# Kernel optimization log

Hardware: AMD Instinct MI355X
Metric: run time of the kernel (lower is better)

The kernel has to match this reference:

```python
import jax, jax.numpy as jnp
import numpy as np

THRESHOLD = 1.25
CURRENT_DECAY = 0.25
VOLTAGE_DECAY = 0.03
B, C_IN, C_HID, C_OUT, T = 16, 64 * 64 * 2, 512, 100, 300


def weight_norm(v, g):
    # per-output-neuron weight normalization: w = g * v / ||v||
    return g[:, None] * v / jnp.linalg.norm(v, axis=1, keepdims=True)


def spike_fn(volt):
    return (volt >= THRESHOLD).astype(volt.dtype)


def lif(z, cd, vd):
    # z: [B, C, T]  CUBA leaky integrate-and-fire recurrence over time
    zT = jnp.moveaxis(z, -1, 0)  # [T, B, C]
    zero = jnp.zeros_like(zT[0])

    def step(carry, zt):
        cur, volt = carry
        cur = (1.0 - cd) * cur + zt
        volt = (1.0 - vd) * volt + cur
        s = spike_fn(volt)
        volt = volt * (1.0 - s)  # reset on spike
        return (cur, volt), s

    _, sT = jax.lax.scan(step, (zero, zero), zT)
    return jnp.moveaxis(sT, 0, -1)  # [B, C, T]


def setup_inputs() -> dict:
    key = jax.random.key(0)
    ks = jax.random.split(key, 8)
    spike = (jax.random.uniform(ks[0], (B, C_IN, T)) < 0.02).astype(jnp.float32)
    s = 0.05
    return {
        "spike": spike,
        "v1": jax.random.normal(ks[1], (C_HID, C_IN), jnp.float32) * s,
        "g1": jnp.ones((C_HID,), jnp.float32),
        "v2": jax.random.normal(ks[2], (C_HID, C_HID), jnp.float32) * s,
        "g2": jnp.ones((C_HID,), jnp.float32),
        "v3": jax.random.normal(ks[3], (C_OUT, C_HID), jnp.float32) * s,
        "g3": jnp.ones((C_OUT,), jnp.float32),
        "current_decays": jnp.full((3,), CURRENT_DECAY, jnp.float32),
        "voltage_decays": jnp.full((3,), VOLTAGE_DECAY, jnp.float32),
    }


def reference(spike, v1, g1, v2, g2, v3, g3, current_decays, voltage_decays):
    x = spike
    for i, (v, g) in enumerate(((v1, g1), (v2, g2), (v3, g3))):
        w = weight_norm(v, g)                      # [out, in]
        z = jnp.einsum("oi,bit->bot", w, x)        # synapse
        x = lif(z, current_decays[i], voltage_decays[i])  # CUBA neuron
    return x
```

## Files before the change

kernel.cpp:

```cpp
#include <hip/hip_runtime.h>
#include <stdint.h>
#include <math.h>

#define NB   16
#define CIN  8192
#define CHID 512
#define COUT 100
#define TT   300
#define TG4  4
#define NTG4 75
#define NW1  256
#define EVCAP1 384
#define EVCAP2 512

__global__ void norm_kernel(const float* __restrict__ v, float* __restrict__ nrm, int cin) {
    int row = blockIdx.x;
    const float* vr = v + (size_t)row * cin;
    float s = 0.f;
    for (int i = threadIdx.x; i < cin; i += 256) {
        float x = vr[i];
        s = __fadd_rn(s, __fmul_rn(x, x));
    }
    __shared__ float red[256];
    red[threadIdx.x] = s;
    __syncthreads();
    for (int off = 128; off > 0; off >>= 1) {
        if (threadIdx.x < off) red[threadIdx.x] += red[threadIdx.x + off];
        __syncthreads();
    }
    if (threadIdx.x == 0) nrm[row] = sqrtf(red[0]);
}

template<int WS>
__global__ void trans_kernel(const float* __restrict__ v, const float* __restrict__ g,
                             const float* __restrict__ nrm, float* __restrict__ wt,
                             int RO, int CI) {
    __shared__ float tile[32][33];
    int i0 = blockIdx.x * 32, o0 = blockIdx.y * 32;
    int tx = threadIdx.x, ty = threadIdx.y;
    for (int k = 0; k < 32; k += 8) {
        int o = o0 + ty + k, i = i0 + tx;
        float val = 0.f;
        if (o < RO) val = __fmul_rn(v[(size_t)o * CI + i], g[o]) / nrm[o];
        tile[ty + k][tx] = val;
    }
    __syncthreads();
    for (int k = 0; k < 32; k += 8) {
        int i = i0 + ty + k, oo = o0 + tx;
        if (oo < WS) wt[(size_t)i * WS + oo] = tile[tx][ty + k];
    }
}

__global__ __launch_bounds__(256) void mask_kernel(const float* __restrict__ spike,
                                                   uint32_t* __restrict__ maskT) {
    __shared__ uint32_t flag[64][16];
    int b = blockIdx.x, itile = blockIdx.y;
    int tid = threadIdx.x;
    int row = tid >> 2, qc = tid & 3;
    const float* sp = spike + ((size_t)(b * CIN + itile * 64 + row)) * TT;
    for (int tc = 0; tc < 5; ++tc) {
        #pragma unroll
        for (int k = 0; k < 4; ++k) {
            int t0 = tc * 64 + k * 16 + qc * 4;
            uint32_t packed = 0;
            if (t0 + 3 < TT) {
                float4 v = *(const float4*)(sp + t0);
                packed = (v.x != 0.f ? 1u : 0u) | (v.y != 0.f ? 0x100u : 0u)
                       | (v.z != 0.f ? 0x10000u : 0u) | (v.w != 0.f ? 0x1000000u : 0u);
            }
            flag[row][k * 4 + qc] = packed;
        }
        __syncthreads();
        if (tid < 128) {
            int t_l = tid >> 1, half = tid & 1;
            int t = tc * 64 + t_l;
            if (t < TT) {
                uint32_t word = 0;
                #pragma unroll
                for (int k = 0; k < 32; ++k) {
                    uint32_t f = flag[half * 32 + k][t_l >> 2];
                    word |= (((f >> ((t_l & 3) * 8)) & 1u) << k);
                }
                maskT[((size_t)b * TT + t) * NW1 + itile * 2 + half] = word;
            }
        }
        __syncthreads();
    }
}

__global__ __launch_bounds__(256) void evmerge1_kernel(const uint32_t* __restrict__ maskT,
                                                       uint32_t* __restrict__ ev,
                                                       int* __restrict__ cnt) {
    int b = blockIdx.x, tg = blockIdx.y;
    int tid = threadIdx.x, lane = tid & 63, wv = tid >> 6;
    int t = tg * TG4 + wv;
    size_t bt = (size_t)b * TT + t;
    const uint32_t* mrow = maskT + bt * NW1;
    uint4 w4 = *(const uint4*)(mrow + lane * 4);
    int c = __popc(w4.x) + __popc(w4.y) + __popc(w4.z) + __popc(w4.w);
    int off = c;
    for (int d = 1; d < 64; d <<= 1) {
        int nn = __shfl_up(off, d, 64);
        if (lane >= d) off += nn;
    }
    int total = __shfl(off, 63, 64);
    off -= c;
    uint32_t* erow = ev + bt * EVCAP1;
    uint32_t wsv[4] = {w4.x, w4.y, w4.z, w4.w};
    int base_i = lane * 128;
    #pragma unroll
    for (int wi = 0; wi < 4; ++wi) {
        uint32_t m = wsv[wi];
        while (m) {
            int bpos = __builtin_ctz(m);
            m &= m - 1;
            if (off < EVCAP1) erow[off] = (uint32_t)(base_i + wi * 32 + bpos) << 11;
            ++off;
        }
    }
    if (lane == 63) cnt[bt] = (total < EVCAP1 ? total : EVCAP1);
}

template<int WS, int EVCAP>
__global__ __launch_bounds__(256) void zg_kernel(const uint32_t* __restrict__ ev,
                                                 const int* __restrict__ cnt,
                                                 const float* __restrict__ wt,
                                                 float* __restrict__ zout) {
    int oslice = blockIdx.x, b = blockIdx.y, tg = blockIdx.z;
    int tid = threadIdx.x, lane = tid & 63, wv = tid >> 6;
    int t = tg * TG4 + wv;
    size_t bt = (size_t)b * TT + t;
    const uint32_t* erow = ev + bt * EVCAP;
    int n = cnt[bt];
    const char* wb = (const char*)wt + (size_t)oslice * 256;
    uint32_t lane4 = (uint32_t)lane * 4u;
    float acc = 0.f;
    int j = 0;
    for (; j + 16 <= n; j += 16) {
        uint4 eA = *(const uint4*)(erow + j);
        uint4 eB = *(const uint4*)(erow + j + 4);
        uint4 eC = *(const uint4*)(erow + j + 8);
        uint4 eD = *(const uint4*)(erow + j + 12);
        float w0  = *(const float*)(wb + (size_t)(eA.x + lane4));
        float w1  = *(const float*)(wb + (size_t)(eA.y + lane4));
        float w2  = *(const float*)(wb + (size_t)(eA.z + lane4));
        float w3  = *(const float*)(wb + (size_t)(eA.w + lane4));
        float w4  = *(const float*)(wb + (size_t)(eB.x + lane4));
        float w5  = *(const float*)(wb + (size_t)(eB.y + lane4));
        float w6  = *(const float*)(wb + (size_t)(eB.z + lane4));
        float w7  = *(const float*)(wb + (size_t)(eB.w + lane4));
        float w8  = *(const float*)(wb + (size_t)(eC.x + lane4));
        float w9  = *(const float*)(wb + (size_t)(eC.y + lane4));
        float w10 = *(const float*)(wb + (size_t)(eC.z + lane4));
        float w11 = *(const float*)(wb + (size_t)(eC.w + lane4));
        float w12 = *(const float*)(wb + (size_t)(eD.x + lane4));
        float w13 = *(const float*)(wb + (size_t)(eD.y + lane4));
        float w14 = *(const float*)(wb + (size_t)(eD.z + lane4));
        float w15 = *(const float*)(wb + (size_t)(eD.w + lane4));
        acc += w0;  acc += w1;  acc += w2;  acc += w3;
        acc += w4;  acc += w5;  acc += w6;  acc += w7;
        acc += w8;  acc += w9;  acc += w10; acc += w11;
        acc += w12; acc += w13; acc += w14; acc += w15;
    }
    for (; j + 4 <= n; j += 4) {
        uint4 e = *(const uint4*)(erow + j);
        float w0 = *(const float*)(wb + (size_t)(e.x + lane4));
        float w1 = *(const float*)(wb + (size_t)(e.y + lane4));
        float w2 = *(const float*)(wb + (size_t)(e.z + lane4));
        float w3 = *(const float*)(wb + (size_t)(e.w + lane4));
        acc += w0; acc += w1; acc += w2; acc += w3;
    }
    for (; j < n; ++j)
        acc += *(const float*)(wb + (size_t)(erow[j] + lane4));
    __builtin_nontemporal_store(acc, zout + bt * WS + oslice * 64 + lane);
}

__global__ __launch_bounds__(64) void lif_ev_kernel(const float* __restrict__ z,
                                                    uint64_t* __restrict__ msk,
                                                    const float* __restrict__ cdarr,
                                                    const float* __restrict__ vdarr,
                                                    int li) {
    int bid = blockIdx.x;
    int b = bid >> 3, oseg = bid & 7;
    int lane = threadIdx.x;
    int o = oseg * 64 + lane;
    float omc = 1.0f - cdarr[li];
    float omv = 1.0f - vdarr[li];
    float cur = 0.f, volt = 0.f;
    const float* zp = z + (size_t)b * TT * CHID + o;

    float A[10], Bv[10];
    auto loadg = [&](float (&buf)[10], int g) {
        #pragma unroll
        for (int k = 0; k < 10; ++k) buf[k] = zp[(size_t)(g * 10 + k) * CHID];
    };
    auto stepg = [&](float (&buf)[10], int g) {
        #pragma unroll
        for (int k = 0; k < 10; ++k) {
            int t = g * 10 + k;
            cur  = __fadd_rn(__fmul_rn(omc, cur), buf[k]);
            volt = __fadd_rn(__fmul_rn(omv, volt), cur);
            bool s = (volt >= 1.25f);
            volt = s ? 0.f : volt;
            uint64_t bal = __ballot(s);
            if (lane == 0) msk[((size_t)b * TT + t) * 8 + oseg] = bal;
        }
    };
    loadg(A, 0);
    for (int g = 0; g < 30; g += 2) {
        if (g + 1 < 30) loadg(Bv, g + 1);
        stepg(A, g);
        if (g + 2 < 30) loadg(A, g + 2);
        if (g + 1 < 30) stepg(Bv, g + 1);
    }
}

__global__ __launch_bounds__(256) void evbuild2_kernel(const uint64_t* __restrict__ msk,
                                                       uint32_t* __restrict__ ev,
                                                       int* __restrict__ cnt, int shift) {
    int b = blockIdx.x, tg = blockIdx.y;
    int tid = threadIdx.x, lane = tid & 63, wv = tid >> 6;
    int t = tg * TG4 + wv;
    size_t bt = (size_t)b * TT + t;
    uint64_t word = msk[bt * 8 + (lane >> 3)];
    uint32_t byte = (uint32_t)(word >> ((lane & 7) * 8)) & 0xFFu;
    int c = __popc(byte);
    int off = c;
    for (int d = 1; d < 64; d <<= 1) {
        int nn = __shfl_up(off, d, 64);
        if (lane >= d) off += nn;
    }
    int total = __shfl(off, 63, 64);
    off -= c;
    uint32_t* erow = ev + bt * EVCAP2;
    int obase = lane * 8;
    while (byte) {
        int k = __builtin_ctz(byte);
        byte &= byte - 1;
        erow[off++] = (uint32_t)(obase + k) << shift;
    }
    if (lane == 63) cnt[bt] = total;
}

__global__ __launch_bounds__(64) void lif_out_kernel(const float* __restrict__ z,
                                                     float* __restrict__ out,
                                                     const float* __restrict__ cdarr,
                                                     const float* __restrict__ vdarr,
                                                     int li) {
    int gid = blockIdx.x * 64 + threadIdx.x;
    if (gid >= NB * COUT) return;
    int b = gid / COUT, o = gid % COUT;
    float omc = 1.0f - cdarr[li];
    float omv = 1.0f - vdarr[li];
    float cur = 0.f, volt = 0.f;
    const float* zp = z + (size_t)b * TT * 128 + o;
    float* op = out + ((size_t)b * COUT + o) * TT;

    float A[10], Bv[10];
    auto loadg = [&](float (&buf)[10], int g) {
        #pragma unroll
        for (int k = 0; k < 10; ++k) buf[k] = zp[(size_t)(g * 10 + k) * 128];
    };
    auto stepg = [&](float (&buf)[10], int g) {
        #pragma unroll
        for (int k = 0; k < 10; ++k) {
            cur  = __fadd_rn(__fmul_rn(omc, cur), buf[k]);
            volt = __fadd_rn(__fmul_rn(omv, volt), cur);
            bool s = (volt >= 1.25f);
            volt = s ? 0.f : volt;
            op[g * 10 + k] = s ? 1.0f : 0.0f;
        }
    };
    loadg(A, 0);
    for (int g = 0; g < 30; g += 2) {
        if (g + 1 < 30) loadg(Bv, g + 1);
        stepg(A, g);
        if (g + 2 < 30) loadg(A, g + 2);
        if (g + 1 < 30) stepg(Bv, g + 1);
    }
}

extern "C" void kernel_launch(void* const* d_in, const int* in_sizes, int n_in,
                              void* d_out, int out_size, void* d_ws, size_t ws_size,
                              hipStream_t stream) {
    const float* spike = (const float*)d_in[0];
    const float* v1 = (const float*)d_in[1];
    const float* g1 = (const float*)d_in[2];
    const float* v2 = (const float*)d_in[3];
    const float* g2 = (const float*)d_in[4];
    const float* v3 = (const float*)d_in[5];
    const float* g3 = (const float*)d_in[6];
    const float* cd = (const float*)d_in[7];
    const float* vd = (const float*)d_in[8];

    float* ws   = (float*)d_ws;
    float* w1t  = ws;
    float* w2t  = w1t + (size_t)CIN * CHID;
    float* w3t  = w2t + (size_t)CHID * CHID;
    float* nrm1 = w3t + (size_t)CHID * 128;
    float* nrm2 = nrm1 + 512;
    float* nrm3 = nrm2 + 512;
    float* zbuf = nrm3 + 128;
    float* z3   = zbuf + (size_t)NB * TT * CHID;
    uint32_t* evb   = (uint32_t*)(z3 + (size_t)NB * TT * 128);
    int*      cntb  = (int*)(evb + (size_t)NB * TT * EVCAP2);
    uint64_t* mskb  = (uint64_t*)(cntb + (size_t)NB * TT);
    uint32_t* maskT = (uint32_t*)(mskb + (size_t)NB * TT * 8);
    size_t need = (size_t)((uint8_t*)(maskT + (size_t)NB * TT * NW1) - (uint8_t*)d_ws);
    if (ws_size < need) return;

    norm_kernel<<<dim3(CHID), dim3(256), 0, stream>>>(v1, nrm1, CIN);
    norm_kernel<<<dim3(CHID), dim3(256), 0, stream>>>(v2, nrm2, CHID);
    norm_kernel<<<dim3(COUT), dim3(256), 0, stream>>>(v3, nrm3, CHID);
    trans_kernel<512><<<dim3(CIN / 32, CHID / 32), dim3(32, 8), 0, stream>>>(v1, g1, nrm1, w1t, CHID, CIN);
    trans_kernel<512><<<dim3(CHID / 32, CHID / 32), dim3(32, 8), 0, stream>>>(v2, g2, nrm2, w2t, CHID, CHID);
    trans_kernel<128><<<dim3(CHID / 32, 4), dim3(32, 8), 0, stream>>>(v3, g3, nrm3, w3t, COUT, CHID);

    mask_kernel<<<dim3(NB, CIN / 64), dim3(256), 0, stream>>>(spike, maskT);
    evmerge1_kernel<<<dim3(NB, NTG4), dim3(256), 0, stream>>>(maskT, evb, cntb);
    zg_kernel<512, EVCAP1><<<dim3(8, NB, NTG4), dim3(256), 0, stream>>>(evb, cntb, w1t, zbuf);
    lif_ev_kernel<<<dim3(NB * 8), dim3(64), 0, stream>>>(zbuf, mskb, cd, vd, 0);
    evbuild2_kernel<<<dim3(NB, NTG4), dim3(256), 0, stream>>>(mskb, evb, cntb, 11);
    zg_kernel<512, EVCAP2><<<dim3(8, NB, NTG4), dim3(256), 0, stream>>>(evb, cntb, w2t, zbuf);
    lif_ev_kernel<<<dim3(NB * 8), dim3(64), 0, stream>>>(zbuf, mskb, cd, vd, 1);
    evbuild2_kernel<<<dim3(NB, NTG4), dim3(256), 0, stream>>>(mskb, evb, cntb, 9);
    zg_kernel<128, EVCAP2><<<dim3(2, NB, NTG4), dim3(256), 0, stream>>>(evb, cntb, w3t, z3);
    lif_out_kernel<<<dim3((NB * COUT + 63) / 64), dim3(64), 0, stream>>>(z3, (float*)d_out, cd, vd, 2);
}
```

Baseline: 251.6 us.

## Fuse event-list building into gather kernels and merge prep launches

```diff
diff --git a/kernel.cpp b/kernel.cpp
--- a/kernel.cpp
+++ b/kernel.cpp
@@ -13,30 +13,96 @@
 #define EVCAP1 384
 #define EVCAP2 512
 
-__global__ void norm_kernel(const float* __restrict__ v, float* __restrict__ nrm, int cin) {
-    int row = blockIdx.x;
-    const float* vr = v + (size_t)row * cin;
-    float s = 0.f;
-    for (int i = threadIdx.x; i < cin; i += 256) {
-        float x = vr[i];
-        s = __fadd_rn(s, __fmul_rn(x, x));
-    }
-    __shared__ float red[256];
-    red[threadIdx.x] = s;
-    __syncthreads();
-    for (int off = 128; off > 0; off >>= 1) {
-        if (threadIdx.x < off) red[threadIdx.x] += red[threadIdx.x + off];
+typedef float fx4 __attribute__((ext_vector_type(4)));
+
+__global__ __launch_bounds__(256) void prep1_kernel(const float* __restrict__ spike,
+                                                    uint32_t* __restrict__ maskT,
+                                                    const float* __restrict__ v1,
+                                                    const float* __restrict__ v2,
+                                                    const float* __restrict__ v3,
+                                                    float* __restrict__ nrm1,
+                                                    float* __restrict__ nrm2,
+                                                    float* __restrict__ nrm3) {
+    int blk = blockIdx.x;
+    int tid = threadIdx.x;
+    if (blk < 2048) {
+        __shared__ uint32_t flag[64][16];
+        int b = blk >> 7, itile = blk & 127;
+        int row = tid >> 2, qc = tid & 3;
+        const float* sp = spike + ((size_t)(b * CIN + itile * 64 + row)) * TT;
+        for (int tc = 0; tc < 5; ++tc) {
+            #pragma unroll
+            for (int k = 0; k < 4; ++k) {
+                int t0 = tc * 64 + k * 16 + qc * 4;
+                uint32_t packed = 0;
+                if (t0 + 3 < TT) {
+                    fx4 v = __builtin_nontemporal_load((const fx4*)(sp + t0));
+                    packed = (v.x != 0.f ? 1u : 0u) | (v.y != 0.f ? 0x100u : 0u)
+                           | (v.z != 0.f ? 0x10000u : 0u) | (v.w != 0.f ? 0x1000000u : 0u);
+                }
+                flag[row][k * 4 + qc] = packed;
+            }
+            __syncthreads();
+            if (tid < 128) {
+                int t_l = tid >> 1, half = tid & 1;
+                int t = tc * 64 + t_l;
+                if (t < TT) {
+                    uint32_t word = 0;
+                    #pragma unroll
+                    for (int k = 0; k < 32; ++k) {
+                        uint32_t f = flag[half * 32 + k][t_l >> 2];
+                        word |= (((f >> ((t_l & 3) * 8)) & 1u) << k);
+                    }
+                    maskT[((size_t)b * TT + t) * NW1 + itile * 2 + half] = word;
+                }
+            }
+            __syncthreads();
+        }
+    } else {
+        int blk2 = blk - 2048;
+        const float* v; float* out; int cin, row;
+        if (blk2 < 512)       { v = v1; out = nrm1; cin = CIN;  row = blk2; }
+        else if (blk2 < 1024) { v = v2; out = nrm2; cin = CHID; row = blk2 - 512; }
+        else                  { v = v3; out = nrm3; cin = CHID; row = blk2 - 1024; }
+        const float* vr = v + (size_t)row * cin;
+        float s = 0.f;
+        for (int i = tid; i < cin; i += 256) {
+            float x = vr[i];
+            s = __fadd_rn(s, __fmul_rn(x, x));
+        }
+        __shared__ float red[256];
+        red[tid] = s;
         __syncthreads();
-    }
-    if (threadIdx.x == 0) nrm[row] = sqrtf(red[0]);
-}
-
-template<int WS>
-__global__ void trans_kernel(const float* __restrict__ v, const float* __restrict__ g,
-                             const float* __restrict__ nrm, float* __restrict__ wt,
-                             int RO, int CI) {
+        for (int off = 128; off > 0; off >>= 1) {
+            if (tid < off) red[tid] += red[tid + off];
+            __syncthreads();
+        }
+        if (tid == 0) out[row] = sqrtf(red[0]);
+    }
+}
+
+__global__ __launch_bounds__(256) void prep2_kernel(
+        const float* __restrict__ v1, const float* __restrict__ g1,
+        const float* __restrict__ nrm1, float* __restrict__ w1t,
+        const float* __restrict__ v2, const float* __restrict__ g2,
+        const float* __restrict__ nrm2, float* __restrict__ w2t,
+        const float* __restrict__ v3, const float* __restrict__ g3,
+        const float* __restrict__ nrm3, float* __restrict__ w3t) {
     __shared__ float tile[32][33];
-    int i0 = blockIdx.x * 32, o0 = blockIdx.y * 32;
+    int blk = blockIdx.x;
+    const float *v, *g, *nrm; float* wt; int CI, RO, WS, i0, o0;
+    if (blk < 4096) {
+        v = v1; g = g1; nrm = nrm1; wt = w1t; CI = CIN; RO = CHID; WS = CHID;
+        i0 = (blk & 255) * 32; o0 = (blk >> 8) * 32;
+    } else if (blk < 4352) {
+        int r = blk - 4096;
+        v = v2; g = g2; nrm = nrm2; wt = w2t; CI = CHID; RO = CHID; WS = CHID;
+        i0 = (r & 15) * 32; o0 = (r >> 4) * 32;
+    } else {
+        int r = blk - 4352;
+        v = v3; g = g3; nrm = nrm3; wt = w3t; CI = CHID; RO = COUT; WS = 128;
+        i0 = (r & 15) * 32; o0 = (r >> 4) * 32;
+    }
     int tx = threadIdx.x, ty = threadIdx.y;
     for (int k = 0; k < 32; k += 8) {
         int o = o0 + ty + k, i = i0 + tx;
@@ -51,96 +117,71 @@
     }
 }
 
-__global__ __launch_bounds__(256) void mask_kernel(const float* __restrict__ spike,
-                                                   uint32_t* __restrict__ maskT) {
-    __shared__ uint32_t flag[64][16];
-    int b = blockIdx.x, itile = blockIdx.y;
-    int tid = threadIdx.x;
-    int row = tid >> 2, qc = tid & 3;
-    const float* sp = spike + ((size_t)(b * CIN + itile * 64 + row)) * TT;
-    for (int tc = 0; tc < 5; ++tc) {
-        #pragma unroll
-        for (int k = 0; k < 4; ++k) {
-            int t0 = tc * 64 + k * 16 + qc * 4;
-            uint32_t packed = 0;
-            if (t0 + 3 < TT) {
-                float4 v = *(const float4*)(sp + t0);
-                packed = (v.x != 0.f ? 1u : 0u) | (v.y != 0.f ? 0x100u : 0u)
-                       | (v.z != 0.f ? 0x10000u : 0u) | (v.w != 0.f ? 0x1000000u : 0u);
-            }
-            flag[row][k * 4 + qc] = packed;
-        }
-        __syncthreads();
-        if (tid < 128) {
-            int t_l = tid >> 1, half = tid & 1;
-            int t = tc * 64 + t_l;
-            if (t < TT) {
-                uint32_t word = 0;
-                #pragma unroll
-                for (int k = 0; k < 32; ++k) {
-                    uint32_t f = flag[half * 32 + k][t_l >> 2];
-                    word |= (((f >> ((t_l & 3) * 8)) & 1u) << k);
-                }
-                maskT[((size_t)b * TT + t) * NW1 + itile * 2 + half] = word;
-            }
-        }
-        __syncthreads();
-    }
-}
-
-__global__ __launch_bounds__(256) void evmerge1_kernel(const uint32_t* __restrict__ maskT,
-                                                       uint32_t* __restrict__ ev,
-                                                       int* __restrict__ cnt) {
-    int b = blockIdx.x, tg = blockIdx.y;
-    int tid = threadIdx.x, lane = tid & 63, wv = tid >> 6;
-    int t = tg * TG4 + wv;
-    size_t bt = (size_t)b * TT + t;
-    const uint32_t* mrow = maskT + bt * NW1;
-    uint4 w4 = *(const uint4*)(mrow + lane * 4);
-    int c = __popc(w4.x) + __popc(w4.y) + __popc(w4.z) + __popc(w4.w);
-    int off = c;
-    for (int d = 1; d < 64; d <<= 1) {
-        int nn = __shfl_up(off, d, 64);
-        if (lane >= d) off += nn;
-    }
-    int total = __shfl(off, 63, 64);
-    off -= c;
-    uint32_t* erow = ev + bt * EVCAP1;
-    uint32_t wsv[4] = {w4.x, w4.y, w4.z, w4.w};
-    int base_i = lane * 128;
-    #pragma unroll
-    for (int wi = 0; wi < 4; ++wi) {
-        uint32_t m = wsv[wi];
-        while (m) {
-            int bpos = __builtin_ctz(m);
-            m &= m - 1;
-            if (off < EVCAP1) erow[off] = (uint32_t)(base_i + wi * 32 + bpos) << 11;
-            ++off;
-        }
-    }
-    if (lane == 63) cnt[bt] = (total < EVCAP1 ? total : EVCAP1);
-}
-
-template<int WS, int EVCAP>
-__global__ __launch_bounds__(256) void zg_kernel(const uint32_t* __restrict__ ev,
-                                                 const int* __restrict__ cnt,
-                                                 const float* __restrict__ wt,
-                                                 float* __restrict__ zout) {
+template<int WS, int EVCAP, int MODE, int SHIFT>
+__global__ __launch_bounds__(256) void zgp_kernel(const void* __restrict__ md,
+                                                  const float* __restrict__ wt,
+                                                  float* __restrict__ zout) {
+    __shared__ alignas(16) uint32_t list[4][EVCAP];
     int oslice = blockIdx.x, b = blockIdx.y, tg = blockIdx.z;
     int tid = threadIdx.x, lane = tid & 63, wv = tid >> 6;
     int t = tg * TG4 + wv;
     size_t bt = (size_t)b * TT + t;
-    const uint32_t* erow = ev + bt * EVCAP;
-    int n = cnt[bt];
+
+    int n;
+    {
+        int c;
+        uint32_t wsv[4]; uint32_t byte = 0;
+        if (MODE == 0) {
+            const uint32_t* mrow = (const uint32_t*)md + bt * NW1;
+            uint4 w4 = *(const uint4*)(mrow + lane * 4);
+            wsv[0] = w4.x; wsv[1] = w4.y; wsv[2] = w4.z; wsv[3] = w4.w;
+            c = __popc(w4.x) + __popc(w4.y) + __popc(w4.z) + __popc(w4.w);
+        } else {
+            const uint64_t* mp = (const uint64_t*)md + bt * 8;
+            uint64_t word = mp[lane >> 3];
+            byte = (uint32_t)(word >> ((lane & 7) * 8)) & 0xFFu;
+            c = __popc(byte);
+        }
+        int off = c;
+        for (int d = 1; d < 64; d <<= 1) {
+            int nn = __shfl_up(off, d, 64);
+            if (lane >= d) off += nn;
+        }
+        int total = __shfl(off, 63, 64);
+        off -= c;
+        if (MODE == 0) {
+            int base_i = lane * 128;
+            #pragma unroll
+            for (int wi = 0; wi < 4; ++wi) {
+                uint32_t m = wsv[wi];
+                while (m) {
+                    int bp = __builtin_ctz(m);
+                    m &= m - 1;
+                    if (off < EVCAP) list[wv][off] = (uint32_t)(base_i + wi * 32 + bp) << SHIFT;
+                    ++off;
+                }
+            }
+        } else {
+            int obase = lane * 8;
+            while (byte) {
+                int k = __builtin_ctz(byte);
+                byte &= byte - 1;
+                list[wv][off++] = (uint32_t)(obase + k) << SHIFT;
+            }
+        }
+        n = total < EVCAP ? total : EVCAP;
+    }
+
+    const uint32_t* lrow = &list[wv][0];
     const char* wb = (const char*)wt + (size_t)oslice * 256;
     uint32_t lane4 = (uint32_t)lane * 4u;
     float acc = 0.f;
     int j = 0;
     for (; j + 16 <= n; j += 16) {
-        uint4 eA = *(const uint4*)(erow + j);
-        uint4 eB = *(const uint4*)(erow + j + 4);
-        uint4 eC = *(const uint4*)(erow + j + 8);
-        uint4 eD = *(const uint4*)(erow + j + 12);
+        uint4 eA = *(const uint4*)(lrow + j);
+        uint4 eB = *(const uint4*)(lrow + j + 4);
+        uint4 eC = *(const uint4*)(lrow + j + 8);
+        uint4 eD = *(const uint4*)(lrow + j + 12);
         float w0  = *(const float*)(wb + (size_t)(eA.x + lane4));
         float w1  = *(const float*)(wb + (size_t)(eA.y + lane4));
         float w2  = *(const float*)(wb + (size_t)(eA.z + lane4));
@@ -163,7 +204,7 @@
         acc += w12; acc += w13; acc += w14; acc += w15;
     }
     for (; j + 4 <= n; j += 4) {
-        uint4 e = *(const uint4*)(erow + j);
+        uint4 e = *(const uint4*)(lrow + j);
         float w0 = *(const float*)(wb + (size_t)(e.x + lane4));
         float w1 = *(const float*)(wb + (size_t)(e.y + lane4));
         float w2 = *(const float*)(wb + (size_t)(e.z + lane4));
@@ -171,8 +212,8 @@
         acc += w0; acc += w1; acc += w2; acc += w3;
     }
     for (; j < n; ++j)
-        acc += *(const float*)(wb + (size_t)(erow[j] + lane4));
-    __builtin_nontemporal_store(acc, zout + bt * WS + oslice * 64 + lane);
+        acc += *(const float*)(wb + (size_t)(lrow[j] + lane4));
+    zout[bt * WS + oslice * 64 + lane] = acc;
 }
 
 __global__ __launch_bounds__(64) void lif_ev_kernel(const float* __restrict__ z,
@@ -215,33 +256,6 @@
     }
 }
 
-__global__ __launch_bounds__(256) void evbuild2_kernel(const uint64_t* __restrict__ msk,
-                                                       uint32_t* __restrict__ ev,
-                                                       int* __restrict__ cnt, int shift) {
-    int b = blockIdx.x, tg = blockIdx.y;
-    int tid = threadIdx.x, lane = tid & 63, wv = tid >> 6;
-    int t = tg * TG4 + wv;
-    size_t bt = (size_t)b * TT + t;
-    uint64_t word = msk[bt * 8 + (lane >> 3)];
-    uint32_t byte = (uint32_t)(word >> ((lane & 7) * 8)) & 0xFFu;
-    int c = __popc(byte);
-    int off = c;
-    for (int d = 1; d < 64; d <<= 1) {
-        int nn = __shfl_up(off, d, 64);
-        if (lane >= d) off += nn;
-    }
-    int total = __shfl(off, 63, 64);
-    off -= c;
-    uint32_t* erow = ev + bt * EVCAP2;
-    int obase = lane * 8;
-    while (byte) {
-        int k = __builtin_ctz(byte);
-        byte &= byte - 1;
-        erow[off++] = (uint32_t)(obase + k) << shift;
-    }
-    if (lane == 63) cnt[bt] = total;
-}
-
 __global__ __launch_bounds__(64) void lif_out_kernel(const float* __restrict__ z,
                                                      float* __restrict__ out,
                                                      const float* __restrict__ cdarr,
@@ -302,28 +316,20 @@
     float* nrm3 = nrm2 + 512;
     float* zbuf = nrm3 + 128;
     float* z3   = zbuf + (size_t)NB * TT * CHID;
-    uint32_t* evb   = (uint32_t*)(z3 + (size_t)NB * TT * 128);
-    int*      cntb  = (int*)(evb + (size_t)NB * TT * EVCAP2);
-    uint64_t* mskb  = (uint64_t*)(cntb + (size_t)NB * TT);
+    uint64_t* mskb  = (uint64_t*)(z3 + (size_t)NB * TT * 128);
     uint32_t* maskT = (uint32_t*)(mskb + (size_t)NB * TT * 8);
     size_t need = (size_t)((uint8_t*)(maskT + (size_t)NB * TT * NW1) - (uint8_t*)d_ws);
     if (ws_size < need) return;
 
-    norm_kernel<<<dim3(CHID), dim3(256), 0, stream>>>(v1, nrm1, CIN);
-    norm_kernel<<<dim3(CHID), dim3(256), 0, stream>>>(v2, nrm2, CHID);
-    norm_kernel<<<dim3(COUT), dim3(256), 0, stream>>>(v3, nrm3, CHID);
-    trans_kernel<512><<<dim3(CIN / 32, CHID / 32), dim3(32, 8), 0, stream>>>(v1, g1, nrm1, w1t, CHID, CIN);
-    trans_kernel<512><<<dim3(CHID / 32, CHID / 32), dim3(32, 8), 0, stream>>>(v2, g2, nrm2, w2t, CHID, CHID);
-    trans_kernel<128><<<dim3(CHID / 32, 4), dim3(32, 8), 0, stream>>>(v3, g3, nrm3, w3t, COUT, CHID);
-
-    mask_kernel<<<dim3(NB, CIN / 64), dim3(256), 0, stream>>>(spike, maskT);
-    evmerge1_kernel<<<dim3(NB, NTG4), dim3(256), 0, stream>>>(maskT, evb, cntb);
-    zg_kernel<512, EVCAP1><<<dim3(8, NB, NTG4), dim3(256), 0, stream>>>(evb, cntb, w1t, zbuf);
+    prep1_kernel<<<dim3(2048 + 1124), dim3(256), 0, stream>>>(spike, maskT, v1, v2, v3,
+                                                              nrm1, nrm2, nrm3);
+    prep2_kernel<<<dim3(4416), dim3(32, 8), 0, stream>>>(v1, g1, nrm1, w1t,
+                                                         v2, g2, nrm2, w2t,
+                                                         v3, g3, nrm3, w3t);
+    zgp_kernel<512, EVCAP1, 0, 11><<<dim3(8, NB, NTG4), dim3(256), 0, stream>>>(maskT, w1t, zbuf);
     lif_ev_kernel<<<dim3(NB * 8), dim3(64), 0, stream>>>(zbuf, mskb, cd, vd, 0);
-    evbuild2_kernel<<<dim3(NB, NTG4), dim3(256), 0, stream>>>(mskb, evb, cntb, 11);
-    zg_kernel<512, EVCAP2><<<dim3(8, NB, NTG4), dim3(256), 0, stream>>>(evb, cntb, w2t, zbuf);
+    zgp_kernel<512, EVCAP2, 1, 11><<<dim3(8, NB, NTG4), dim3(256), 0, stream>>>(mskb, w2t, zbuf);
     lif_ev_kernel<<<dim3(NB * 8), dim3(64), 0, stream>>>(zbuf, mskb, cd, vd, 1);
-    evbuild2_kernel<<<dim3(NB, NTG4), dim3(256), 0, stream>>>(mskb, evb, cntb, 9);
-    zg_kernel<128, EVCAP2><<<dim3(2, NB, NTG4), dim3(256), 0, stream>>>(evb, cntb, w3t, z3);
+    zgp_kernel<128, EVCAP2, 1, 9><<<dim3(2, NB, NTG4), dim3(256), 0, stream>>>(mskb, w3t, z3);
     lif_out_kernel<<<dim3((NB * COUT + 63) / 64), dim3(64), 0, stream>>>(z3, (float*)d_out, cd, vd, 2);
 }
```

Result: faster. 201.3 us (-20.0%).
